# Kernel optimization log

Hardware: AMD Instinct MI355X
Metric: run time of the kernel (lower is better)

The kernel has to match this reference:

```python
import jax, jax.numpy as jnp
import numpy as np

N_NODES = 100000
N_EDGES = 1600000
IN_DIM = 512
OUT_DIM = 64


def setup_inputs() -> dict:
    key = jax.random.key(0)
    k1, k2, k3 = jax.random.split(key, 3)
    x = jax.random.normal(k1, (N_NODES, IN_DIM), dtype=jnp.float32)
    edge_index = jax.random.randint(k2, (2, N_EDGES), 0, N_NODES, dtype=jnp.int64)
    # Glorot-ish init for the GCNConv linear weight, stored as [in, out]
    W = jax.random.normal(k3, (IN_DIM, OUT_DIM), dtype=jnp.float32) * (1.0 / np.sqrt(IN_DIM))
    b = jnp.zeros((OUT_DIM,), dtype=jnp.float32)
    return {"x": x, "edge_index": edge_index, "W": W, "b": b}


def reference(x, edge_index, W, b):
    N = x.shape[0]
    # --- gcn_norm: add self-loops, symmetric degree normalization ---
    loop = jnp.arange(N, dtype=edge_index.dtype)
    src = jnp.concatenate([edge_index[0], loop])  # message sources
    dst = jnp.concatenate([edge_index[1], loop])  # aggregation targets
    deg = jax.ops.segment_sum(jnp.ones_like(dst, dtype=x.dtype), dst, num_segments=N)
    deg_inv_sqrt = jnp.where(deg > 0, jax.lax.rsqrt(jnp.maximum(deg, 1.0)), 0.0)
    norm = deg_inv_sqrt[src] * deg_inv_sqrt[dst]  # [E+N]
    # --- linear transform then gather-scale-scatter aggregation ---
    h = x @ W                                   # [N, out]
    msg = h[src] * norm[:, None]                # [E+N, out]
    out = jax.ops.segment_sum(msg, dst, num_segments=N) + b
    return jax.nn.log_softmax(out, axis=1)
```

## Files before the change

kernel.cpp:

```cpp
#include <hip/hip_runtime.h>
#include <math.h>

#define N_NODES 100000
#define N_EDGES 1600000
#define IN_DIM 512
#define OUT_DIM 64
#define SCAN_CHUNK 1024
#define N_SCAN_BLOCKS ((N_NODES + SCAN_CHUNK - 1) / SCAN_CHUNK)
#define N_TILES (N_NODES / 16)

typedef __attribute__((ext_vector_type(8))) short short8;
typedef __attribute__((ext_vector_type(4))) float float4v;

__device__ __forceinline__ unsigned short f2bf(float f) {
    unsigned int u = __float_as_uint(f);
    u += 0x7fffu + ((u >> 16) & 1u);
    return (unsigned short)(u >> 16);
}
__device__ __forceinline__ float bf2f(unsigned short s) {
    return __uint_as_float(((unsigned int)s) << 16);
}

__global__ __launch_bounds__(256) void k_zero(int* __restrict__ degi) {
    int i = blockIdx.x * 256 + threadIdx.x;
    if (i < N_NODES) degi[i] = 0;
}

__global__ __launch_bounds__(256) void k_count(const int* __restrict__ dst,
                                               int* __restrict__ degi) {
    int e = blockIdx.x * 256 + threadIdx.x;
    if (e < N_EDGES) atomicAdd(&degi[dst[e]], 1);
}

__global__ __launch_bounds__(256) void k_scan1(const int* __restrict__ degi,
                                               int* __restrict__ row_ptr,
                                               int* __restrict__ blockSums) {
    __shared__ int wsum[4];
    const int t = threadIdx.x, lane = t & 63, w = t >> 6;
    const int i = (blockIdx.x * 256 + t) * 4;
    int d[4];
#pragma unroll
    for (int j = 0; j < 4; ++j) d[j] = (i + j < N_NODES) ? degi[i + j] : 0;
    int tsum = d[0] + d[1] + d[2] + d[3];
    int incl = tsum;
#pragma unroll
    for (int off = 1; off < 64; off <<= 1) {
        int v = __shfl_up(incl, off, 64);
        if (lane >= off) incl += v;
    }
    if (lane == 63) wsum[w] = incl;
    __syncthreads();
    int woff = 0;
#pragma unroll
    for (int k = 0; k < 4; ++k) if (k < w) woff += wsum[k];
    int excl = woff + incl - tsum;
    if (i < N_NODES) {
        int run = excl;
#pragma unroll
        for (int j = 0; j < 4; ++j) {
            if (i + j < N_NODES) row_ptr[i + j] = run;
            run += d[j];
        }
    }
    __syncthreads();
    if (t == 0) blockSums[blockIdx.x] = wsum[0] + wsum[1] + wsum[2] + wsum[3];
}

__global__ __launch_bounds__(128) void k_scan2(const int* __restrict__ blockSums,
                                               int* __restrict__ blockOffsets) {
    __shared__ int s[128];
    int t = threadIdx.x;
    int v = (t < N_SCAN_BLOCKS) ? blockSums[t] : 0;
    s[t] = v;
    __syncthreads();
#pragma unroll
    for (int off = 1; off < 128; off <<= 1) {
        int add = (t >= off) ? s[t - off] : 0;
        __syncthreads();
        s[t] += add;
        __syncthreads();
    }
    if (t < N_SCAN_BLOCKS) blockOffsets[t] = s[t] - v;
}

__global__ __launch_bounds__(256) void k_scan3(int* __restrict__ row_ptr,
                                               const int* __restrict__ blockOffsets,
                                               int* __restrict__ csr_pos) {
    int i = blockIdx.x * 256 + threadIdx.x;
    if (i < N_NODES) {
        int v = row_ptr[i] + blockOffsets[i >> 10];
        row_ptr[i] = v;
        csr_pos[i] = v;
    }
}

__global__ __launch_bounds__(256) void k_fill(const int* __restrict__ src,
                                              const int* __restrict__ dst,
                                              int* __restrict__ csr_pos,
                                              int* __restrict__ csr) {
    int e = blockIdx.x * 256 + threadIdx.x;
    if (e < N_EDGES) {
        int pos = atomicAdd(&csr_pos[dst[e]], 1);
        csr[pos] = src[e];
    }
}

__global__ __launch_bounds__(256) void k_wswz(const float* __restrict__ W,
                                              unsigned short* __restrict__ Wswz) {
    int t = blockIdx.x * 256 + threadIdx.x;
    if (t < IN_DIM * OUT_DIM) {
        int k = t >> 6, n = t & 63;
        int kt = k >> 5, kin = k & 31;
        int quad = kin >> 3, j = kin & 7;
        int ct = n >> 4, l16 = n & 15;
        int lane = quad * 16 + l16;
        Wswz[(((kt * 4 + ct) * 64 + lane) * 8) + j] = f2bf(W[t]);
    }
}

__global__ __launch_bounds__(256) void k_gemm(const float* __restrict__ x,
                                              const unsigned short* __restrict__ Wswz,
                                              const int* __restrict__ degi,
                                              unsigned short* __restrict__ h) {
    __shared__ short8 Wlds[64][64];
    const int t = threadIdx.x;
    {
        const float4v* s = (const float4v*)Wswz;
        float4v* d = (float4v*)Wlds;
        for (int i = t; i < 4096; i += 256) d[i] = s[i];
    }
    __syncthreads();

    const int lane = t & 63;
    const int quad = lane >> 4, l16 = lane & 15;
    const int gw = blockIdx.x * 4 + (t >> 6);
    const int nw = gridDim.x * 4;

    for (int tile = gw; tile < N_TILES; tile += nw) {
        const int r0 = tile * 16;
        const float* xrow = x + (size_t)(r0 + l16) * IN_DIM + quad * 8;
        float4v a[32];
#pragma unroll
        for (int kt = 0; kt < 16; ++kt) {
            a[kt * 2 + 0] = *(const float4v*)(xrow + kt * 32);
            a[kt * 2 + 1] = *(const float4v*)(xrow + kt * 32 + 4);
        }
        float4v acc[4] = {{0.f,0.f,0.f,0.f},{0.f,0.f,0.f,0.f},
                          {0.f,0.f,0.f,0.f},{0.f,0.f,0.f,0.f}};
#pragma unroll
        for (int kt = 0; kt < 16; ++kt) {
            union { short8 s8; unsigned short us[8]; } af;
            float4v lo = a[kt * 2], hi = a[kt * 2 + 1];
            af.us[0] = f2bf(lo.x); af.us[1] = f2bf(lo.y);
            af.us[2] = f2bf(lo.z); af.us[3] = f2bf(lo.w);
            af.us[4] = f2bf(hi.x); af.us[5] = f2bf(hi.y);
            af.us[6] = f2bf(hi.z); af.us[7] = f2bf(hi.w);
#pragma unroll
            for (int ct = 0; ct < 4; ++ct) {
                short8 bf = Wlds[kt * 4 + ct][lane];
                acc[ct] = __builtin_amdgcn_mfma_f32_16x16x32_bf16(af.s8, bf, acc[ct], 0, 0, 0);
            }
        }
#pragma unroll
        for (int reg = 0; reg < 4; ++reg) {
            int orow = r0 + quad * 4 + reg;
            float dinv = rsqrtf((float)(degi[orow] + 1));
#pragma unroll
            for (int ct = 0; ct < 4; ++ct)
                h[(size_t)orow * OUT_DIM + ct * 16 + l16] = f2bf(acc[ct][reg] * dinv);
        }
    }
}

__global__ __launch_bounds__(256) void k_gather(const int* __restrict__ degi,
                                                const int* __restrict__ row_ptr,
                                                const int* __restrict__ csr,
                                                const unsigned short* __restrict__ h,
                                                const float* __restrict__ b,
                                                float* __restrict__ out) {
    int node = blockIdx.x * 4 + (threadIdx.x >> 6);
    int lane = threadIdx.x & 63;
    if (node >= N_NODES) return;
    int cnt  = __builtin_amdgcn_readfirstlane(degi[node]);
    int base = __builtin_amdgcn_readfirstlane(row_ptr[node]);

    float acc = bf2f(h[(size_t)node * OUT_DIM + lane]);
    int e = 0;
    for (; e + 8 <= cnt; e += 8) {
        int s0 = csr[base + e + 0], s1 = csr[base + e + 1];
        int s2 = csr[base + e + 2], s3 = csr[base + e + 3];
        int s4 = csr[base + e + 4], s5 = csr[base + e + 5];
        int s6 = csr[base + e + 6], s7 = csr[base + e + 7];
        float v0 = bf2f(h[(size_t)s0 * OUT_DIM + lane]);
        float v1 = bf2f(h[(size_t)s1 * OUT_DIM + lane]);
        float v2 = bf2f(h[(size_t)s2 * OUT_DIM + lane]);
        float v3 = bf2f(h[(size_t)s3 * OUT_DIM + lane]);
        float v4 = bf2f(h[(size_t)s4 * OUT_DIM + lane]);
        float v5 = bf2f(h[(size_t)s5 * OUT_DIM + lane]);
        float v6 = bf2f(h[(size_t)s6 * OUT_DIM + lane]);
        float v7 = bf2f(h[(size_t)s7 * OUT_DIM + lane]);
        acc += ((v0 + v1) + (v2 + v3)) + ((v4 + v5) + (v6 + v7));
    }
    for (; e < cnt; ++e)
        acc += bf2f(h[(size_t)csr[base + e] * OUT_DIM + lane]);

    float v = acc * rsqrtf((float)(cnt + 1)) + b[lane];
    float m = v;
#pragma unroll
    for (int off = 32; off > 0; off >>= 1) m = fmaxf(m, __shfl_xor(m, off, 64));
    float ex = expf(v - m);
    float s = ex;
#pragma unroll
    for (int off = 32; off > 0; off >>= 1) s += __shfl_xor(s, off, 64);
    out[(size_t)node * OUT_DIM + lane] = v - m - logf(s);
}

extern "C" void kernel_launch(void* const* d_in, const int* in_sizes, int n_in,
                              void* d_out, int out_size, void* d_ws, size_t ws_size,
                              hipStream_t stream) {
    const float* x  = (const float*)d_in[0];
    const int*   ei = (const int*)d_in[1];
    const float* W  = (const float*)d_in[2];
    const float* b  = (const float*)d_in[3];
    float* out = (float*)d_out;

    char* ws = (char*)d_ws;
    int*            degi         = (int*)(ws + 0);
    int*            csr_pos      = (int*)(ws + 400000);
    int*            row_ptr      = (int*)(ws + 800000);
    int*            blockSums    = (int*)(ws + 1200000);
    int*            blockOffsets = (int*)(ws + 1200512);
    unsigned short* Wswz         = (unsigned short*)(ws + 1201024);
    unsigned short* h            = (unsigned short*)(ws + 1266560);
    int*            csr          = (int*)(ws + 14066560);

    const int* src = ei;
    const int* dst = ei + N_EDGES;

    k_zero  <<<(N_NODES + 255) / 256, 256, 0, stream>>>(degi);
    k_count <<<(N_EDGES + 255) / 256, 256, 0, stream>>>(dst, degi);
    k_scan1 <<<N_SCAN_BLOCKS,         256, 0, stream>>>(degi, row_ptr, blockSums);
    k_scan2 <<<1,                     128, 0, stream>>>(blockSums, blockOffsets);
    k_scan3 <<<(N_NODES + 255) / 256, 256, 0, stream>>>(row_ptr, blockOffsets, csr_pos);
    k_fill  <<<(N_EDGES + 255) / 256, 256, 0, stream>>>(src, dst, csr_pos, csr);
    k_wswz  <<<(IN_DIM * OUT_DIM + 255) / 256, 256, 0, stream>>>(W, Wswz);
    k_gemm  <<<512,                   256, 0, stream>>>(x, Wswz, degi, h);
    k_gather<<<(N_NODES + 3) / 4,     256, 0, stream>>>(degi, row_ptr, csr, h, b, out);
}
```

Before: 564.0 us.

## Build CSR via two-level bucketed counting sort with LDS atomics

Replaces the global-atomic degree count, three-kernel scan and atomic scatter fill with a two-pass radix-style partition: per-block LDS histograms over 1024 coarse buckets, a single-block offset computation, a partition of edges into buckets, then a per-bucket local sort that produces degrees, row pointers and CSR. This is meant to cut contended global atomics and random scattered writes by keeping atomics in shared memory and making the final writes local to each bucket. In exchange, only 128 blocks run the histogram and partition passes and the offsets step is serial over those blocks on a single workgroup. Source and local node ids are packed into one int, which relies on fixed node-count limits.

```diff
diff --git a/kernel.cpp b/kernel.cpp
--- a/kernel.cpp
+++ b/kernel.cpp
@@ -5,8 +5,10 @@
 #define N_EDGES 1600000
 #define IN_DIM 512
 #define OUT_DIM 64
-#define SCAN_CHUNK 1024
-#define N_SCAN_BLOCKS ((N_NODES + SCAN_CHUNK - 1) / SCAN_CHUNK)
+#define NB 1024
+#define NPB 128
+#define CHUNK (N_EDGES / NPB)
+#define N_BUCKETS_USED 782
 #define N_TILES (N_NODES / 16)
 
 typedef __attribute__((ext_vector_type(8))) short short8;
@@ -21,87 +23,125 @@
     return __uint_as_float(((unsigned int)s) << 16);
 }
 
-__global__ __launch_bounds__(256) void k_zero(int* __restrict__ degi) {
-    int i = blockIdx.x * 256 + threadIdx.x;
-    if (i < N_NODES) degi[i] = 0;
-}
-
-__global__ __launch_bounds__(256) void k_count(const int* __restrict__ dst,
-                                               int* __restrict__ degi) {
-    int e = blockIdx.x * 256 + threadIdx.x;
-    if (e < N_EDGES) atomicAdd(&degi[dst[e]], 1);
-}
-
-__global__ __launch_bounds__(256) void k_scan1(const int* __restrict__ degi,
-                                               int* __restrict__ row_ptr,
-                                               int* __restrict__ blockSums) {
-    __shared__ int wsum[4];
+__global__ __launch_bounds__(256) void k_hist1(const int* __restrict__ dst,
+                                               int* __restrict__ blockHist) {
+    __shared__ int hist[NB];
+    const int t = threadIdx.x, b = blockIdx.x;
+    for (int k = t; k < NB; k += 256) hist[k] = 0;
+    __syncthreads();
+    const int e0 = b * CHUNK;
+    for (int i = t; i < CHUNK; i += 256)
+        atomicAdd(&hist[dst[e0 + i] >> 7], 1);
+    __syncthreads();
+    for (int k = t; k < NB; k += 256) blockHist[b * NB + k] = hist[k];
+}
+
+__global__ __launch_bounds__(256) void k_offsets(const int* __restrict__ blockHist,
+                                                 int* __restrict__ blockStart,
+                                                 int* __restrict__ bucketBase) {
+    __shared__ int colsum[NB];
+    __shared__ int bbase[NB + 1];
+    __shared__ int wtot[4];
     const int t = threadIdx.x, lane = t & 63, w = t >> 6;
-    const int i = (blockIdx.x * 256 + t) * 4;
-    int d[4];
-#pragma unroll
-    for (int j = 0; j < 4; ++j) d[j] = (i + j < N_NODES) ? degi[i + j] : 0;
-    int tsum = d[0] + d[1] + d[2] + d[3];
+    for (int k = t; k < NB; k += 256) {
+        int s = 0;
+        for (int b = 0; b < NPB; ++b) s += blockHist[b * NB + k];
+        colsum[k] = s;
+    }
+    __syncthreads();
+    int c0 = colsum[t * 4 + 0], c1 = colsum[t * 4 + 1];
+    int c2 = colsum[t * 4 + 2], c3 = colsum[t * 4 + 3];
+    int tsum = c0 + c1 + c2 + c3;
     int incl = tsum;
 #pragma unroll
     for (int off = 1; off < 64; off <<= 1) {
-        int v = __shfl_up(incl, off, 64);
-        if (lane >= off) incl += v;
-    }
-    if (lane == 63) wsum[w] = incl;
+        int u = __shfl_up(incl, off, 64);
+        if (lane >= off) incl += u;
+    }
+    if (lane == 63) wtot[w] = incl;
     __syncthreads();
     int woff = 0;
 #pragma unroll
-    for (int k = 0; k < 4; ++k) if (k < w) woff += wsum[k];
+    for (int k2 = 0; k2 < 4; ++k2) if (k2 < w) woff += wtot[k2];
     int excl = woff + incl - tsum;
-    if (i < N_NODES) {
-        int run = excl;
-#pragma unroll
-        for (int j = 0; j < 4; ++j) {
-            if (i + j < N_NODES) row_ptr[i + j] = run;
-            run += d[j];
-        }
-    }
-    __syncthreads();
-    if (t == 0) blockSums[blockIdx.x] = wsum[0] + wsum[1] + wsum[2] + wsum[3];
-}
-
-__global__ __launch_bounds__(128) void k_scan2(const int* __restrict__ blockSums,
-                                               int* __restrict__ blockOffsets) {
-    __shared__ int s[128];
-    int t = threadIdx.x;
-    int v = (t < N_SCAN_BLOCKS) ? blockSums[t] : 0;
-    s[t] = v;
-    __syncthreads();
-#pragma unroll
-    for (int off = 1; off < 128; off <<= 1) {
-        int add = (t >= off) ? s[t - off] : 0;
-        __syncthreads();
-        s[t] += add;
-        __syncthreads();
-    }
-    if (t < N_SCAN_BLOCKS) blockOffsets[t] = s[t] - v;
-}
-
-__global__ __launch_bounds__(256) void k_scan3(int* __restrict__ row_ptr,
-                                               const int* __restrict__ blockOffsets,
-                                               int* __restrict__ csr_pos) {
-    int i = blockIdx.x * 256 + threadIdx.x;
-    if (i < N_NODES) {
-        int v = row_ptr[i] + blockOffsets[i >> 10];
-        row_ptr[i] = v;
-        csr_pos[i] = v;
-    }
-}
-
-__global__ __launch_bounds__(256) void k_fill(const int* __restrict__ src,
-                                              const int* __restrict__ dst,
-                                              int* __restrict__ csr_pos,
-                                              int* __restrict__ csr) {
-    int e = blockIdx.x * 256 + threadIdx.x;
-    if (e < N_EDGES) {
-        int pos = atomicAdd(&csr_pos[dst[e]], 1);
-        csr[pos] = src[e];
+    bbase[t * 4 + 0] = excl;
+    bbase[t * 4 + 1] = excl + c0;
+    bbase[t * 4 + 2] = excl + c0 + c1;
+    bbase[t * 4 + 3] = excl + c0 + c1 + c2;
+    if (t == 255) bbase[NB] = excl + tsum;
+    __syncthreads();
+    for (int k = t; k < NB + 1; k += 256) bucketBase[k] = bbase[k];
+    for (int k = t; k < NB; k += 256) {
+        int run = bbase[k];
+        for (int b = 0; b < NPB; ++b) {
+            blockStart[b * NB + k] = run;
+            run += blockHist[b * NB + k];
+        }
+    }
+}
+
+__global__ __launch_bounds__(256) void k_partition(const int* __restrict__ dst,
+                                                   const int* __restrict__ src,
+                                                   const int* __restrict__ blockStart,
+                                                   int* __restrict__ parts) {
+    __shared__ int cursor[NB];
+    const int t = threadIdx.x, b = blockIdx.x;
+    for (int k = t; k < NB; k += 256) cursor[k] = blockStart[b * NB + k];
+    __syncthreads();
+    const int e0 = b * CHUNK;
+    for (int i = t; i < CHUNK; i += 256) {
+        int d = dst[e0 + i];
+        int s = src[e0 + i];
+        int k = d >> 7;
+        int pos = atomicAdd(&cursor[k], 1);
+        parts[pos] = ((d & 127) << 17) | s;
+    }
+}
+
+__global__ __launch_bounds__(256) void k_bucket(const int* __restrict__ parts,
+                                                const int* __restrict__ bucketBase,
+                                                int* __restrict__ degi,
+                                                int* __restrict__ row_ptr,
+                                                int* __restrict__ csr) {
+    __shared__ int cnt[128];
+    __shared__ int cur[128];
+    __shared__ int wtot[2];
+    const int t = threadIdx.x, k = blockIdx.x;
+    const int base = bucketBase[k];
+    const int n    = bucketBase[k + 1] - base;
+    if (t < 128) cnt[t] = 0;
+    __syncthreads();
+    for (int i = t; i < n; i += 256)
+        atomicAdd(&cnt[parts[base + i] >> 17], 1);
+    __syncthreads();
+    int incl = 0, v = 0;
+    if (t < 128) {
+        int lane = t & 63;
+        v = cnt[t];
+        incl = v;
+#pragma unroll
+        for (int off = 1; off < 64; off <<= 1) {
+            int u = __shfl_up(incl, off, 64);
+            if (lane >= off) incl += u;
+        }
+        if (lane == 63) wtot[t >> 6] = incl;
+    }
+    __syncthreads();
+    if (t < 128) {
+        int excl = incl - v + ((t >> 6) ? wtot[0] : 0);
+        cur[t] = excl;
+        int node = k * 128 + t;
+        if (node < N_NODES) {
+            degi[node]    = v;
+            row_ptr[node] = base + excl;
+        }
+    }
+    __syncthreads();
+    for (int i = t; i < n; i += 256) {
+        int code = parts[base + i];
+        int nl = code >> 17, s = code & 0x1FFFF;
+        int pos = atomicAdd(&cur[nl], 1);
+        csr[base + pos] = s;
     }
 }
 
@@ -225,25 +265,24 @@
     float* out = (float*)d_out;
 
     char* ws = (char*)d_ws;
-    int*            degi         = (int*)(ws + 0);
-    int*            csr_pos      = (int*)(ws + 400000);
-    int*            row_ptr      = (int*)(ws + 800000);
-    int*            blockSums    = (int*)(ws + 1200000);
-    int*            blockOffsets = (int*)(ws + 1200512);
-    unsigned short* Wswz         = (unsigned short*)(ws + 1201024);
-    unsigned short* h            = (unsigned short*)(ws + 1266560);
-    int*            csr          = (int*)(ws + 14066560);
+    int*            degi       = (int*)(ws + 0);
+    int*            row_ptr    = (int*)(ws + 400000);
+    int*            blockHist  = (int*)(ws + 800000);
+    int*            blockStart = (int*)(ws + 1324288);
+    int*            bucketBase = (int*)(ws + 1848576);
+    unsigned short* Wswz       = (unsigned short*)(ws + 1852928);
+    unsigned short* h          = (unsigned short*)(ws + 1918464);
+    int*            parts      = (int*)(ws + 14718464);
+    int*            csr        = (int*)(ws + 21118464);
 
     const int* src = ei;
     const int* dst = ei + N_EDGES;
 
-    k_zero  <<<(N_NODES + 255) / 256, 256, 0, stream>>>(degi);
-    k_count <<<(N_EDGES + 255) / 256, 256, 0, stream>>>(dst, degi);
-    k_scan1 <<<N_SCAN_BLOCKS,         256, 0, stream>>>(degi, row_ptr, blockSums);
-    k_scan2 <<<1,                     128, 0, stream>>>(blockSums, blockOffsets);
-    k_scan3 <<<(N_NODES + 255) / 256, 256, 0, stream>>>(row_ptr, blockOffsets, csr_pos);
-    k_fill  <<<(N_EDGES + 255) / 256, 256, 0, stream>>>(src, dst, csr_pos, csr);
-    k_wswz  <<<(IN_DIM * OUT_DIM + 255) / 256, 256, 0, stream>>>(W, Wswz);
-    k_gemm  <<<512,                   256, 0, stream>>>(x, Wswz, degi, h);
-    k_gather<<<(N_NODES + 3) / 4,     256, 0, stream>>>(degi, row_ptr, csr, h, b, out);
-}
+    k_hist1    <<<NPB, 256, 0, stream>>>(dst, blockHist);
+    k_offsets  <<<1,   256, 0, stream>>>(blockHist, blockStart, bucketBase);
+    k_partition<<<NPB, 256, 0, stream>>>(dst, src, blockStart, parts);
+    k_bucket   <<<N_BUCKETS_USED, 256, 0, stream>>>(parts, bucketBase, degi, row_ptr, csr);
+    k_wswz     <<<(IN_DIM * OUT_DIM + 255) / 256, 256, 0, stream>>>(W, Wswz);
+    k_gemm     <<<512, 256, 0, stream>>>(x, Wswz, degi, h);
+    k_gather   <<<(N_NODES + 3) / 4, 256, 0, stream>>>(degi, row_ptr, csr, h, b, out);
+}
```

Result: faster. 484.5 us (-14.1%).
